# Optimization experiments

Measured on AMD Instinct MI355X. Metric: run time of the kernel, lower is better.

The kernel has to match this reference:

```python
import math
import jax, jax.numpy as jnp
import numpy as np

B, N, H, D = 2, 2048, 16, 64


def _build_idx_table(seq_len, is_causal=True):
    """Fused hierarchical lookup table, faithful to
    build_hierarchical_index_lookup_table. Returns int32 [seq_len, log2(N)+1].
    Entries are (node_index + 1), negated if causally masked.
    Node numbering: leaves 0..N-1, then each level's parents appended;
    parent(i) = i // 2 + seq_len.
    """
    assert seq_len & (seq_len - 1) == 0
    total_nodes = 2 * seq_len - 1
    max_valid = total_nodes - 2  # root is never a neighbor
    level_num = int(math.log2(seq_len))
    total_cols = level_num + 1
    idx = np.ones((seq_len, total_cols), dtype=np.int32)
    n_cur = np.arange(seq_len, dtype=np.int64)
    idx[:, 0] = (n_cur + 1).astype(np.int32)  # self leaf
    for lvl in range(1, total_cols):
        if lvl == 1:
            n_next = n_cur ^ 1          # sibling leaf
            pair = n_cur
        else:
            pair = n_cur // 2 + seq_len  # parent node
            n_next = pair ^ 1            # uncle node
        valid = n_next <= max_valid
        val = n_next + 1
        if is_causal:
            should_mask = (pair < n_next) & valid
            val = np.where(should_mask, -val, val)
        idx[:, lvl] = np.where(valid, val.astype(np.int32), idx[:, lvl])
        n_cur = n_next
    return idx


IDX_TABLE = _build_idx_table(N, is_causal=True)  # [N, LEVELS]


def setup_inputs() -> dict:
    key = jax.random.key(0)
    kq, kk, kv = jax.random.split(key, 3)
    Q = jax.random.normal(kq, (B, N, H, D), dtype=jnp.float32)
    K = jax.random.normal(kk, (B, N, H, D), dtype=jnp.float32)
    V = jax.random.normal(kv, (B, N, H, D), dtype=jnp.float32)
    return {"Q": Q, "K": K, "V": V}


def _build_tree(K, V, scale):
    """Build the full binary-tree node set [B, 2N-1, H, D] for K and V.
    Each parent is a 3-way attention mix of {parent-mean, child0, child1}
    (build_parent_nodes semantics: fp32 online softmax with +1e-9 in denom),
    with the same weights applied to K and V values."""
    Ks, Vs = [K], [V]
    Kc, Vc = K, V
    while Kc.shape[1] > 1:  # trace-time loop over log2(N) levels
        K0, K1 = Kc[:, 0::2], Kc[:, 1::2]
        V0, V1 = Vc[:, 0::2], Vc[:, 1::2]
        Kp0 = 0.5 * (K0 + K1)  # initial parent K (query)
        Vp0 = 0.5 * (V0 + V1)
        s_self = jnp.sum(Kp0 * Kp0, axis=-1) * scale  # [B,P,H]
        s0 = jnp.sum(Kp0 * K0, axis=-1) * scale
        s1 = jnp.sum(Kp0 * K1, axis=-1) * scale
        m = jnp.maximum(s_self, jnp.maximum(s0, s1))
        e_s, e0, e1 = jnp.exp(s_self - m), jnp.exp(s0 - m), jnp.exp(s1 - m)
        denom = e_s + e0 + e1 + 1e-9
        ws, w0, w1 = (e_s / denom)[..., None], (e0 / denom)[..., None], (e1 / denom)[..., None]
        Kc = ws * Kp0 + w0 * K0 + w1 * K1
        Vc = ws * Vp0 + w0 * V0 + w1 * V1
        Ks.append(Kc)
        Vs.append(Vc)
    return jnp.concatenate(Ks, axis=1), jnp.concatenate(Vs, axis=1)


def reference(Q, K, V):
    b, n, h, d = Q.shape
    scale = 1.0 / math.sqrt(d)
    K_all, V_all = _build_tree(K, V, scale)  # [B, 2N-1, H, D]

    raw = jnp.asarray(IDX_TABLE)             # [N, L], sign-encoded
    nbr = jnp.abs(raw) - 1                   # neighbor node indices
    masked = raw < 0                         # causal mask

    Kg = jnp.take(K_all, nbr, axis=1)        # [B, N, L, H, D]
    Vg = jnp.take(V_all, nbr, axis=1)

    scores = jnp.einsum('bnhd,bnlhd->bnhl', Q, Kg) * scale
    scores = jnp.where(masked[None, :, None, :], -jnp.inf, scores)
    w = jax.nn.softmax(scores, axis=-1)      # [B, N, H, L]
    out = jnp.einsum('bnhl,bnlhd->bnhd', w, Vg)
    return out
```

## Files before the change

### kernel.cpp

```cpp
#include <hip/hip_runtime.h>

#define NSEQ   2048
#define HEADS  16
#define DIM    64
#define BATCH  2
#define SCALE  0.125f

#define WSSLOTS 2048
#define ROWF4   (DIM / 4)
#define HSTRIDE (HEADS * ROWF4)
#define KVBYTES ((size_t)BATCH * WSSLOTS * HEADS * 256)

__device__ __forceinline__ int level_offset(int j) {
    return (j == 0) ? 0 : (2 * NSEQ - ((2 * NSEQ) >> j));
}

__device__ __forceinline__ float dot4(float4 a, float4 b) {
    return a.x * b.x + a.y * b.y + a.z * b.z + a.w * b.w;
}

template <int CTRL>
__device__ __forceinline__ float dpp_radd(float x) {
    int y = __builtin_amdgcn_update_dpp(0, __float_as_int(x), CTRL, 0xF, 0xF, true);
    return x + __int_as_float(y);
}
__device__ __forceinline__ float rsum16(float x) {
    x = dpp_radd<0xB1>(x);
    x = dpp_radd<0x4E>(x);
    x = dpp_radd<0x141>(x);
    x = dpp_radd<0x140>(x);
    return x;
}

__device__ __forceinline__ unsigned short bf16rne(float x) {
    unsigned u = __float_as_uint(x);
    return (unsigned short)((u + 0x7FFFu + ((u >> 16) & 1u)) >> 16);
}
__device__ __forceinline__ unsigned pack2(float a, float b) {
    return (unsigned)bf16rne(a) | ((unsigned)bf16rne(b) << 16);
}
__device__ __forceinline__ uint4 packKV(float4 k, float4 v) {
    return make_uint4(pack2(k.x, k.y), pack2(k.z, k.w),
                      pack2(v.x, v.y), pack2(v.z, v.w));
}
__device__ __forceinline__ float2 unpack2(unsigned u) {
    return make_float2(__uint_as_float(u << 16),
                       __uint_as_float(u & 0xFFFF0000u));
}
__device__ __forceinline__ float4 unpackK(uint4 p) {
    float2 a = unpack2(p.x), b = unpack2(p.y);
    return make_float4(a.x, a.y, b.x, b.y);
}
__device__ __forceinline__ float4 unpackV(uint4 p) {
    float2 a = unpack2(p.z), b = unpack2(p.w);
    return make_float4(a.x, a.y, b.x, b.y);
}

__device__ __forceinline__ void reduce3_16(float& a, float& b, float& c) {
    a = rsum16(a);
    b = rsum16(b);
    c = rsum16(c);
}

__device__ __forceinline__ void reduce6_16(float& a, float& b, float& c,
                                           float& d, float& e, float& f) {
    a = rsum16(a);
    b = rsum16(b);
    c = rsum16(c);
    d = rsum16(d);
    e = rsum16(e);
    f = rsum16(f);
}

__device__ __forceinline__ void make_parent4(float4 k0, float4 k1, float4 v0, float4 v1,
                                             float4& kc, float4& vc) {
    float4 kp, vp;
    kp.x = 0.5f * (k0.x + k1.x); kp.y = 0.5f * (k0.y + k1.y);
    kp.z = 0.5f * (k0.z + k1.z); kp.w = 0.5f * (k0.w + k1.w);
    vp.x = 0.5f * (v0.x + v1.x); vp.y = 0.5f * (v0.y + v1.y);
    vp.z = 0.5f * (v0.z + v1.z); vp.w = 0.5f * (v0.w + v1.w);
    float ss = dot4(kp, kp), sa = dot4(kp, k0), sb = dot4(kp, k1);
    reduce3_16(ss, sa, sb);
    ss *= SCALE; sa *= SCALE; sb *= SCALE;
    float mx = fmaxf(ss, fmaxf(sa, sb));
    float es = __expf(ss - mx), ea = __expf(sa - mx), eb = __expf(sb - mx);
    float inv = 1.0f / (es + ea + eb + 1e-9f);
    es *= inv; ea *= inv; eb *= inv;
    kc.x = es * kp.x + ea * k0.x + eb * k1.x;
    kc.y = es * kp.y + ea * k0.y + eb * k1.y;
    kc.z = es * kp.z + ea * k0.z + eb * k1.z;
    kc.w = es * kp.w + ea * k0.w + eb * k1.w;
    vc.x = es * vp.x + ea * v0.x + eb * v1.x;
    vc.y = es * vp.y + ea * v0.y + eb * v1.y;
    vc.z = es * vp.z + ea * v0.z + eb * v1.z;
    vc.w = es * vp.w + ea * v0.w + eb * v1.w;
}

__device__ __forceinline__ void make_parent_pair4(const float4* k, const float4* v,
                                                  float4& ka, float4& va,
                                                  float4& kb, float4& vb) {
    float4 kpa, vpa, kpb, vpb;
    kpa.x = 0.5f * (k[0].x + k[1].x); kpa.y = 0.5f * (k[0].y + k[1].y);
    kpa.z = 0.5f * (k[0].z + k[1].z); kpa.w = 0.5f * (k[0].w + k[1].w);
    vpa.x = 0.5f * (v[0].x + v[1].x); vpa.y = 0.5f * (v[0].y + v[1].y);
    vpa.z = 0.5f * (v[0].z + v[1].z); vpa.w = 0.5f * (v[0].w + v[1].w);
    kpb.x = 0.5f * (k[2].x + k[3].x); kpb.y = 0.5f * (k[2].y + k[3].y);
    kpb.z = 0.5f * (k[2].z + k[3].z); kpb.w = 0.5f * (k[2].w + k[3].w);
    vpb.x = 0.5f * (v[2].x + v[3].x); vpb.y = 0.5f * (v[2].y + v[3].y);
    vpb.z = 0.5f * (v[2].z + v[3].z); vpb.w = 0.5f * (v[2].w + v[3].w);
    float ssa = dot4(kpa, kpa), saa = dot4(kpa, k[0]), sba = dot4(kpa, k[1]);
    float ssb = dot4(kpb, kpb), sab = dot4(kpb, k[2]), sbb = dot4(kpb, k[3]);
    reduce6_16(ssa, saa, sba, ssb, sab, sbb);
    ssa *= SCALE; saa *= SCALE; sba *= SCALE;
    ssb *= SCALE; sab *= SCALE; sbb *= SCALE;
    float mxa = fmaxf(ssa, fmaxf(saa, sba));
    float mxb = fmaxf(ssb, fmaxf(sab, sbb));
    float esa = __expf(ssa - mxa), eaa = __expf(saa - mxa), eba = __expf(sba - mxa);
    float esb = __expf(ssb - mxb), eab = __expf(sab - mxb), ebb = __expf(sbb - mxb);
    float iva = 1.0f / (esa + eaa + eba + 1e-9f);
    float ivb = 1.0f / (esb + eab + ebb + 1e-9f);
    esa *= iva; eaa *= iva; eba *= iva;
    esb *= ivb; eab *= ivb; ebb *= ivb;
    ka.x = esa * kpa.x + eaa * k[0].x + eba * k[1].x;
    ka.y = esa * kpa.y + eaa * k[0].y + eba * k[1].y;
    ka.z = esa * kpa.z + eaa * k[0].z + eba * k[1].z;
    ka.w = esa * kpa.w + eaa * k[0].w + eba * k[1].w;
    va.x = esa * vpa.x + eaa * v[0].x + eba * v[1].x;
    va.y = esa * vpa.y + eaa * v[0].y + eba * v[1].y;
    va.z = esa * vpa.z + eaa * v[0].z + eba * v[1].z;
    va.w = esa * vpa.w + eaa * v[0].w + eba * v[1].w;
    kb.x = esb * kpb.x + eab * k[2].x + ebb * k[3].x;
    kb.y = esb * kpb.y + eab * k[2].y + ebb * k[3].y;
    kb.z = esb * kpb.z + eab * k[2].z + ebb * k[3].z;
    kb.w = esb * kpb.w + eab * k[2].w + ebb * k[3].w;
    vb.x = esb * vpb.x + eab * v[2].x + ebb * v[3].x;
    vb.y = esb * vpb.y + eab * v[2].y + ebb * v[3].y;
    vb.z = esb * vpb.z + eab * v[2].z + ebb * v[3].z;
    vb.w = esb * vpb.w + eab * v[2].w + ebb * v[3].w;
}

__device__ __forceinline__ void quad_step(const float4* k, const float4* v,
                                          uint4* KVw,
                                          size_t pRow0, size_t gRow,
                                          int t,
                                          float4& kg, float4& vg) {
    float4 ka, va, kb, vb;
    make_parent_pair4(k, v, ka, va, kb, vb);
    KVw[pRow0 + t] = packKV(ka, va);
    KVw[pRow0 + HSTRIDE + t] = packKV(kb, vb);
    make_parent4(ka, kb, va, vb, kg, vg);
    KVw[gRow + t] = packKV(kg, vg);
}

__global__ __launch_bounds__(256) void tree_low(const float* __restrict__ K,
                                                const float* __restrict__ V,
                                                uint4* __restrict__ KVw,
                                                float* __restrict__ Kw6,
                                                float* __restrict__ Vw6) {
    __shared__ float4 Kb[20 * ROWF4];
    __shared__ float4 Vb[20 * ROWF4];
    const float4* K4 = (const float4*)K;
    const float4* V4 = (const float4*)V;
    float4* Kw6f = (float4*)Kw6;
    float4* Vw6f = (float4*)Vw6;

    int bid = blockIdx.x;
    int c = bid & 31;
    int h = (bid >> 5) & 15;
    int b = bid >> 9;
    int lane = threadIdx.x & 63;
    int gg = (threadIdx.x >> 6) * 4 + (lane >> 4);
    int t = lane & 15;

    size_t wsBase = (size_t)(b * WSSLOTS) * HSTRIDE + h * ROWF4;

    {
        int n0 = c * 64 + 4 * gg;
        const float4* Kr = K4 + ((size_t)((b * NSEQ + n0) * HEADS + h)) * ROWF4;
        const float4* Vr = V4 + ((size_t)((b * NSEQ + n0) * HEADS + h)) * ROWF4;
        float4 k[4], v[4];
#pragma unroll
        for (int j = 0; j < 4; ++j) { k[j] = Kr[j * HSTRIDE + t]; v[j] = Vr[j * HSTRIDE + t]; }
        int s1 = c * 32 + 2 * gg;
        int s2 = 1024 + c * 16 + gg;
        float4 kg, vg;
        quad_step(k, v, KVw, wsBase + (size_t)s1 * HSTRIDE,
                  wsBase + (size_t)s2 * HSTRIDE, t, kg, vg);
        Kb[gg * ROWF4 + t] = kg;  Vb[gg * ROWF4 + t] = vg;
    }
    __syncthreads();
    if (gg < 4) {
        float4 k[4], v[4];
#pragma unroll
        for (int j = 0; j < 4; ++j) {
            k[j] = Kb[(4 * gg + j) * ROWF4 + t];
            v[j] = Vb[(4 * gg + j) * ROWF4 + t];
        }
        int s3 = 1536 + c * 8 + 2 * gg;
        int s4 = 1792 + c * 4 + gg;
        float4 kg, vg;
        quad_step(k, v, KVw, wsBase + (size_t)s3 * HSTRIDE,
                  wsBase + (size_t)s4 * HSTRIDE, t, kg, vg);
        Kb[(16 + gg) * ROWF4 + t] = kg;  Vb[(16 + gg) * ROWF4 + t] = vg;
    }
    __syncthreads();
    if (gg == 0) {
        float4 k[4], v[4];
#pragma unroll
        for (int j = 0; j < 4; ++j) {
            k[j] = Kb[(16 + j) * ROWF4 + t];
            v[j] = Vb[(16 + j) * ROWF4 + t];
        }
        int s5 = 1920 + c * 2;
        int s6 = 1984 + c;
        float4 kg, vg;
        quad_step(k, v, KVw, wsBase + (size_t)s5 * HSTRIDE,
                  wsBase + (size_t)s6 * HSTRIDE, t, kg, vg);
        size_t st = ((size_t)((b * 32 + c) * HEADS + h)) * ROWF4 + t;
        Kw6f[st] = kg;  Vw6f[st] = vg;
    }
}

__global__ __launch_bounds__(256) void tree_top(uint4* __restrict__ KVw,
                                                const float* __restrict__ Kw6,
                                                const float* __restrict__ Vw6) {
    __shared__ float4 Kb[8 * ROWF4];
    __shared__ float4 Vb[8 * ROWF4];
    const float4* Kw6f = (const float4*)Kw6;
    const float4* Vw6f = (const float4*)Vw6;

    int h = blockIdx.x & 15, b = blockIdx.x >> 4;
    int lane = threadIdx.x & 63;
    int gg = (threadIdx.x >> 6) * 4 + (lane >> 4);
    int t = lane & 15;
    size_t wsBase = (size_t)(b * WSSLOTS) * HSTRIDE + h * ROWF4;

    if (gg < 8) {
        float4 k[4], v[4];
#pragma unroll
        for (int j = 0; j < 4; ++j) {
            size_t r = ((size_t)((b * 32 + 4 * gg + j) * HEADS + h)) * ROWF4 + t;
            k[j] = Kw6f[r]; v[j] = Vw6f[r];
        }
        int s7 = 2016 + 2 * gg;
        int s8 = 2032 + gg;
        float4 kg, vg;
        quad_step(k, v, KVw, wsBase + (size_t)s7 * HSTRIDE,
                  wsBase + (size_t)s8 * HSTRIDE, t, kg, vg);
        Kb[gg * ROWF4 + t] = kg;  Vb[gg * ROWF4 + t] = vg;
    }
    __syncthreads();
    if (gg < 2) {
        float4 k[4], v[4];
#pragma unroll
        for (int j = 0; j < 4; ++j) {
            k[j] = Kb[(4 * gg + j) * ROWF4 + t];
            v[j] = Vb[(4 * gg + j) * ROWF4 + t];
        }
        int s9  = 2040 + 2 * gg;
        int s10 = 2044 + gg;
        float4 kg, vg;
        quad_step(k, v, KVw, wsBase + (size_t)s9 * HSTRIDE,
                  wsBase + (size_t)s10 * HSTRIDE, t, kg, vg);
    }
}

__global__ __launch_bounds__(256) void attn(const float* __restrict__ Q,
                                            const float* __restrict__ K,
                                            const float* __restrict__ V,
                                            const uint4* __restrict__ KVw,
                                            float* __restrict__ out) {
    const float4* Q4 = (const float4*)Q;
    const float4* K4 = (const float4*)K;
    const float4* V4 = (const float4*)V;
    float4* O4 = (float4*)out;

    int bid = blockIdx.x;
    int vbid = ((bid & 7) << 9) | (bid >> 3);
    int w = vbid * 4 + (threadIdx.x >> 6);
    int lane = threadIdx.x & 63;
    int g = lane >> 4;
    int t = lane & 15;
    int h = (w & 3) * 4 + g;
    int n = (w >> 2) & (NSEQ - 1);
    int b = w >> 13;

    int row0 = (b * NSEQ + n) * HSTRIDE;
    int row1 = (b * NSEQ + (n ^ 1)) * HSTRIDE;
    int rowt[10];
#pragma unroll
    for (int l = 2; l < 12; ++l) {
        int j = l - 1;
        int slot = level_offset(j) - NSEQ + ((n >> j) ^ 1);
        rowt[l - 2] = (b * WSSLOTS + slot) * HSTRIDE;
    }
    int hoff = h * ROWF4 + t;

    unsigned active = 1u | (((unsigned)n & 0x7FFu) << 1);
    active = (unsigned)__builtin_amdgcn_readfirstlane((int)active);

    float4 q4 = Q4[row0 + hoff];
    q4.x *= SCALE; q4.y *= SCALE; q4.z *= SCALE; q4.w *= SCALE;

    float4 k0 = K4[row0 + hoff];
    float4 v0 = V4[row0 + hoff];
    float4 k1, v1;
    if (active & 2u) { k1 = K4[row1 + hoff]; v1 = V4[row1 + hoff]; }
    uint4 kv[10];
#pragma unroll
    for (int l = 2; l < 12; ++l)
        if (active & (1u << l)) kv[l - 2] = KVw[rowt[l - 2] + hoff];

    float s[12];
    s[0] = dot4(q4, k0);
    s[1] = (active & 2u) ? dot4(q4, k1) : 0.f;
#pragma unroll
    for (int l = 2; l < 12; ++l)
        s[l] = (active & (1u << l)) ? dot4(q4, unpackK(kv[l - 2])) : 0.f;

#pragma unroll
    for (int l = 0; l < 12; ++l)
        if (active & (1u << l)) s[l] = rsum16(s[l]);

    float mx = -3.402823466e+38f;
#pragma unroll
    for (int l = 0; l < 12; ++l)
        if (active & (1u << l)) mx = fmaxf(mx, s[l]);
    float sum = 0.f;
#pragma unroll
    for (int l = 0; l < 12; ++l) {
        float e = (active & (1u << l)) ? __expf(s[l] - mx) : 0.f;
        s[l] = e;
        sum += e;
    }
    float inv = 1.0f / sum;

    float4 o = make_float4(0.f, 0.f, 0.f, 0.f);
    o.x += s[0] * v0.x; o.y += s[0] * v0.y;
    o.z += s[0] * v0.z; o.w += s[0] * v0.w;
    if (active & 2u) {
        o.x += s[1] * v1.x; o.y += s[1] * v1.y;
        o.z += s[1] * v1.z; o.w += s[1] * v1.w;
    }
#pragma unroll
    for (int l = 2; l < 12; ++l) {
        if (active & (1u << l)) {
            float4 vv = unpackV(kv[l - 2]);
            o.x += s[l] * vv.x; o.y += s[l] * vv.y;
            o.z += s[l] * vv.z; o.w += s[l] * vv.w;
        }
    }
    O4[row0 + hoff] = make_float4(o.x * inv, o.y * inv, o.z * inv, o.w * inv);
}

extern "C" void kernel_launch(void* const* d_in, const int* in_sizes, int n_in,
                              void* d_out, int out_size, void* d_ws, size_t ws_size,
                              hipStream_t stream) {
    const float* Q = (const float*)d_in[0];
    const float* K = (const float*)d_in[1];
    const float* V = (const float*)d_in[2];
    float* out = (float*)d_out;
    uint4* KVw = (uint4*)d_ws;
    float* Kw6 = (float*)((char*)d_ws + KVBYTES);
    float* Vw6 = Kw6 + (size_t)BATCH * 32 * HEADS * DIM;

    tree_low<<<1024, 256, 0, stream>>>(K, V, KVw, Kw6, Vw6);
    tree_top<<<BATCH * HEADS, 256, 0, stream>>>(KVw, Kw6, Vw6);
    attn<<<(BATCH * NSEQ * (HEADS / 4)) / 4, 256, 0, stream>>>(Q, K, V, KVw, out);
}
```

Before: 113.3 us.

## Pair sibling queries per wavefront and share leaf K/V via lane shuffle

Remaps the attention kernel so that each wavefront handles two sibling tokens (n, n^1) across two heads, instead of one token across four heads. The sibling leaf K/V is then fetched with a cross-lane shuffle rather than a second global load. Because siblings share the same ancestor nodes, their tree-node loads can also hit the same cache lines. The costs are eight extra shuffles per thread and a per-half-wave select for the causal sibling mask; the active-level mask stays wave-uniform because it depends only on the pair index.

```diff
diff --git a/kernel.cpp b/kernel.cpp
--- a/kernel.cpp
+++ b/kernel.cpp
@@ -279,14 +279,16 @@
     int vbid = ((bid & 7) << 9) | (bid >> 3);
     int w = vbid * 4 + (threadIdx.x >> 6);
     int lane = threadIdx.x & 63;
-    int g = lane >> 4;
+    int g2 = lane >> 5;
+    int hh = (lane >> 4) & 1;
     int t = lane & 15;
-    int h = (w & 3) * 4 + g;
-    int n = (w >> 2) & (NSEQ - 1);
-    int b = w >> 13;
+    int hp = w & 7;
+    int p  = (w >> 3) & 1023;
+    int b  = w >> 13;
+    int n  = 2 * p + g2;
+    int h  = 2 * hp + hh;
 
     int row0 = (b * NSEQ + n) * HSTRIDE;
-    int row1 = (b * NSEQ + (n ^ 1)) * HSTRIDE;
     int rowt[10];
 #pragma unroll
     for (int l = 2; l < 12; ++l) {
@@ -296,7 +298,7 @@
     }
     int hoff = h * ROWF4 + t;
 
-    unsigned active = 1u | (((unsigned)n & 0x7FFu) << 1);
+    unsigned active = 1u | (((unsigned)p & 0x3FFu) << 2);
     active = (unsigned)__builtin_amdgcn_readfirstlane((int)active);
 
     float4 q4 = Q4[row0 + hoff];
@@ -304,44 +306,57 @@
 
     float4 k0 = K4[row0 + hoff];
     float4 v0 = V4[row0 + hoff];
-    float4 k1, v1;
-    if (active & 2u) { k1 = K4[row1 + hoff]; v1 = V4[row1 + hoff]; }
     uint4 kv[10];
 #pragma unroll
     for (int l = 2; l < 12; ++l)
         if (active & (1u << l)) kv[l - 2] = KVw[rowt[l - 2] + hoff];
 
+    float4 ks, vs;
+    ks.x = __shfl_xor(k0.x, 32, 64); ks.y = __shfl_xor(k0.y, 32, 64);
+    ks.z = __shfl_xor(k0.z, 32, 64); ks.w = __shfl_xor(k0.w, 32, 64);
+    vs.x = __shfl_xor(v0.x, 32, 64); vs.y = __shfl_xor(v0.y, 32, 64);
+    vs.z = __shfl_xor(v0.z, 32, 64); vs.w = __shfl_xor(v0.w, 32, 64);
+
     float s[12];
     s[0] = dot4(q4, k0);
-    s[1] = (active & 2u) ? dot4(q4, k1) : 0.f;
+    s[1] = dot4(q4, ks);
 #pragma unroll
     for (int l = 2; l < 12; ++l)
         s[l] = (active & (1u << l)) ? dot4(q4, unpackK(kv[l - 2])) : 0.f;
 
-#pragma unroll
-    for (int l = 0; l < 12; ++l)
+    s[0] = rsum16(s[0]);
+    s[1] = rsum16(s[1]);
+#pragma unroll
+    for (int l = 2; l < 12; ++l)
         if (active & (1u << l)) s[l] = rsum16(s[l]);
 
-    float mx = -3.402823466e+38f;
-#pragma unroll
-    for (int l = 0; l < 12; ++l)
+    float mx = s[0];
+    mx = fmaxf(mx, g2 ? s[1] : -3.402823466e+38f);
+#pragma unroll
+    for (int l = 2; l < 12; ++l)
         if (active & (1u << l)) mx = fmaxf(mx, s[l]);
-    float sum = 0.f;
-#pragma unroll
-    for (int l = 0; l < 12; ++l) {
+
+    float sum;
+    {
+        float e0 = __expf(s[0] - mx);
+        float e1 = __expf(s[1] - mx);
+        e1 = g2 ? e1 : 0.f;
+        s[0] = e0; s[1] = e1;
+        sum = e0 + e1;
+    }
+#pragma unroll
+    for (int l = 2; l < 12; ++l) {
         float e = (active & (1u << l)) ? __expf(s[l] - mx) : 0.f;
         s[l] = e;
         sum += e;
     }
     float inv = 1.0f / sum;
 
-    float4 o = make_float4(0.f, 0.f, 0.f, 0.f);
-    o.x += s[0] * v0.x; o.y += s[0] * v0.y;
-    o.z += s[0] * v0.z; o.w += s[0] * v0.w;
-    if (active & 2u) {
-        o.x += s[1] * v1.x; o.y += s[1] * v1.y;
-        o.z += s[1] * v1.z; o.w += s[1] * v1.w;
-    }
+    float4 o;
+    o.x = s[0] * v0.x + s[1] * vs.x;
+    o.y = s[0] * v0.y + s[1] * vs.y;
+    o.z = s[0] * v0.z + s[1] * vs.z;
+    o.w = s[0] * v0.w + s[1] * vs.w;
 #pragma unroll
     for (int l = 2; l < 12; ++l) {
         if (active & (1u << l)) {
@@ -366,5 +381,5 @@
 
     tree_low<<<1024, 256, 0, stream>>>(K, V, KVw, Kw6, Vw6);
     tree_top<<<BATCH * HEADS, 256, 0, stream>>>(KVw, Kw6, Vw6);
-    attn<<<(BATCH * NSEQ * (HEADS / 4)) / 4, 256, 0, stream>>>(Q, K, V, KVw, out);
-}
+    attn<<<(BATCH * (NSEQ / 2) * (HEADS / 2)) / 4, 256, 0, stream>>>(Q, K, V, KVw, out);
+}
```

Result: faster. 110.0 us (-2.9%).
